# Optimization experiments

Hardware: AMD Instinct MI355X
Metric: run time of the kernel (lower is better)

Reference implementation:

```python
import jax, jax.numpy as jnp
import numpy as np

B = 32768      # batch
D = 2          # input_dim
H = 2048       # hidden_dim
NQ = 4         # qubits


def setup_inputs() -> dict:
    key = jax.random.key(0)
    ks = jax.random.split(key, 14)

    def lin(k, fan_in, fan_out):
        # kaiming-uniform-ish init like nn.Linear
        bound = 1.0 / np.sqrt(fan_in)
        kw, kb = jax.random.split(k)
        W = jax.random.uniform(kw, (fan_in, fan_out), jnp.float32, -bound, bound)
        b = jax.random.uniform(kb, (fan_out,), jnp.float32, -bound, bound)
        return W, b

    x = jax.random.normal(ks[0], (B, D), jnp.float32)
    W1, b1 = lin(ks[1], D + NQ, H)      # core Linear 1
    W2, b2 = lin(ks[2], H, H)           # core Linear 2
    Wc, bc = lin(ks[3], H, 1)           # classifier
    Wr1, br1 = lin(ks[4], D, 8)
    Wr2, br2 = lin(ks[5], 8, 4)
    Wr3, br3 = lin(ks[6], 4, 1)
    return dict(x=x, W1=W1, b1=b1, W2=W2, b2=b2, Wc=Wc, bc=bc,
                Wr1=Wr1, br1=br1, Wr2=Wr2, br2=br2, Wr3=Wr3, br3=br3)


def _quantum_feature_map(x):
    # Exact closed form of: RY(x_i) on 4 qubits from |0000>, CNOT(0,1), CNOT(2,3),
    # expval(PauliZ(i)). Padding with zeros -> cos(0)=1 on unused wires.
    xq = jnp.pad(x, ((0, 0), (0, NQ - x.shape[1])))  # [B,4]
    c = jnp.cos(xq)
    return jnp.stack([c[:, 0], c[:, 0] * c[:, 1], c[:, 2], c[:, 2] * c[:, 3]], axis=1)


def reference(x, W1, b1, W2, b2, Wc, bc, Wr1, br1, Wr2, br2, Wr3, br3):
    qfeat = _quantum_feature_map(x)               # [B,4]
    concat = jnp.concatenate([x, qfeat], axis=1)  # [B, D+4]
    h = jnp.tanh(concat @ W1 + b1)                # [B,H]
    h = jnp.tanh(h @ W2 + b2)                     # [B,H]
    logits = h @ Wc + bc                          # [B,1]
    r = jnp.tanh(x @ Wr1 + br1)
    r = jnp.tanh(r @ Wr2 + br2)
    risk = r @ Wr3 + br3                          # [B,1]
    return logits, risk
```

## Files before the change

kernel.cpp:

```cpp
#include <hip/hip_runtime.h>
#include <hip/hip_bf16.h>
#include <stdint.h>

#define B_ROWS 32768
#define HID    2048
#define K_DIM  2048

#define BM 128
#define BN 256
#define BKB 128

#define SCALE_W   5747.3639f
#define DEQUANT   1.3700225e-6f

#define L1_BLOCKS (B_ROWS / 32)
#define TR_BLOCKS ((HID/32)*(K_DIM/32))

typedef int  int4v __attribute__((ext_vector_type(4)));
typedef char char8 __attribute__((ext_vector_type(8)));

__device__ __forceinline__ float fast_tanh(float x) {
    float e = __expf(2.0f * x);
    return 1.0f - 2.0f * __builtin_amdgcn_rcpf(e + 1.0f);
}

__device__ __forceinline__ void gl_lds16(const void* g, void* l) {
    __builtin_amdgcn_global_load_lds(
        (const __attribute__((address_space(1))) void*)(uintptr_t)g,
        (__attribute__((address_space(3))) void*)(uint32_t)(uintptr_t)l,
        16, 0, 0);
}

__global__ __launch_bounds__(256) void prep_kernel(
    const float* __restrict__ x,   const float* __restrict__ W1, const float* __restrict__ b1,
    const float* __restrict__ W2,
    const float* __restrict__ Wr1, const float* __restrict__ br1,
    const float* __restrict__ Wr2, const float* __restrict__ br2,
    const float* __restrict__ Wr3, const float* __restrict__ br3,
    const float* __restrict__ bc,
    char* __restrict__ h1, char* __restrict__ W2t, float* __restrict__ out) {
    const int t = threadIdx.x;
    if (blockIdx.x >= L1_BLOCKS) {
        __shared__ float tile[32][33];
        const int tb = blockIdx.x - L1_BLOCKS;
        const int n0 = (tb & 63) * 32;
        const int k0 = (tb >> 6) * 32;
        const int tx = t & 31;
        const int ty = t >> 5;
#pragma unroll
        for (int i = 0; i < 4; ++i) {
            int k = k0 + ty + i * 8;
            tile[ty + i * 8][tx] = W2[(size_t)k * HID + n0 + tx];
        }
        __syncthreads();
#pragma unroll
        for (int i = 0; i < 4; ++i) {
            int n = n0 + ty + i * 8;
            W2t[(size_t)n * K_DIM + k0 + tx] =
                (char)__float2int_rn(tile[tx][ty + i * 8] * SCALE_W);
        }
        return;
    }
    __shared__ float4 xsh[32];
    const int brow0 = blockIdx.x * 32;
    if (t < 32) {
        const float2 xv = *(const float2*)(x + 2 * (brow0 + t));
        const float c0 = __cosf(xv.x);
        xsh[t] = float4{xv.x, xv.y, c0, c0 * __cosf(xv.y)};
    }
    const int n0 = t * 8;
    float w0[8], w1[8], w2[8], w3[8], wb[8];
#pragma unroll
    for (int j = 0; j < 8; ++j) {
        w0[j] = W1[0 * HID + n0 + j];
        w1[j] = W1[1 * HID + n0 + j];
        w2[j] = W1[2 * HID + n0 + j];
        w3[j] = W1[3 * HID + n0 + j];
        wb[j] = W1[4 * HID + n0 + j] + W1[5 * HID + n0 + j] + b1[n0 + j];
    }
    __syncthreads();
#pragma unroll 2
    for (int r = 0; r < 32; ++r) {
        const float4 xr = xsh[r];
        char8 v;
#pragma unroll
        for (int j = 0; j < 8; ++j) {
            float z = wb[j] + xr.x * w0[j] + xr.y * w1[j] + xr.z * w2[j] + xr.w * w3[j];
            v[j] = (char)__float2int_rn(fast_tanh(z) * 127.0f);
        }
        *(char8*)(h1 + (size_t)(brow0 + r) * HID + n0) = v;
    }
    if (t < 32) {
        const float x0 = xsh[t].x, x1 = xsh[t].y;
        float r1[8];
#pragma unroll
        for (int j = 0; j < 8; ++j)
            r1[j] = fast_tanh(br1[j] + x0 * Wr1[j] + x1 * Wr1[8 + j]);
        float r2[4];
#pragma unroll
        for (int j = 0; j < 4; ++j) {
            float s = br2[j];
#pragma unroll
            for (int i = 0; i < 8; ++i) s += r1[i] * Wr2[i * 4 + j];
            r2[j] = fast_tanh(s);
        }
        float risk = br3[0];
#pragma unroll
        for (int i = 0; i < 4; ++i) risk += r2[i] * Wr3[i];
        out[B_ROWS + brow0 + t] = risk;
        out[brow0 + t]          = bc[0];
    }
}

__global__ __launch_bounds__(256, 2) void gemm_kernel(
    const char* __restrict__ A,
    const char* __restrict__ Bt,
    const float* __restrict__ b2, const float* __restrict__ Wc,
    float* __restrict__ out) {
    __shared__ __align__(16) char sA[BM * BKB];
    __shared__ __align__(16) char sB[BN * BKB];

    const int tid  = threadIdx.x;
    const int wave = tid >> 6;
    const int lane = tid & 63;
    const int bid  = blockIdx.x;
    const int m0 = (bid >> 3) * BM;
    const int n0 = (bid & 7) * BN;

    const char* aSrc[4]; char* aDst[4];
    const char* bSrc[8]; char* bDst[8];
    {
        const int rsub  = lane >> 3;
        const int chunk = (lane & 7) ^ rsub;
#pragma unroll
        for (int i = 0; i < 4; ++i) {
            int seg = wave * 4 + i;
            aSrc[i] = A + (size_t)(m0 + seg * 8 + rsub) * K_DIM + chunk * 16;
            aDst[i] = sA + seg * 1024;
        }
#pragma unroll
        for (int i = 0; i < 8; ++i) {
            int seg = wave * 8 + i;
            bSrc[i] = Bt + (size_t)(n0 + seg * 8 + rsub) * K_DIM + chunk * 16;
            bDst[i] = sB + seg * 1024;
        }
    }

    int4v acc[4][8] = {};
    const int mw   = (wave & 1) * 64;
    const int nw   = (wave >> 1) * 128;
    const int quad = lane >> 4;
    const int r16  = lane & 15;
    const int x7   = lane & 7;

    for (int kb = 0; kb < K_DIM; kb += BKB) {
#pragma unroll
        for (int i = 0; i < 4; ++i) gl_lds16(aSrc[i] + kb, aDst[i]);
#pragma unroll
        for (int i = 0; i < 8; ++i) gl_lds16(bSrc[i] + kb, bDst[i]);
        __syncthreads();
#pragma unroll
        for (int ks = 0; ks < 2; ++ks) {
            const int slot = ((ks * 4 + quad) ^ x7) * 16;
            int4v af[4], bfr[8];
#pragma unroll
            for (int mi = 0; mi < 4; ++mi)
                af[mi]  = *(const int4v*)(sA + (mw + mi * 16 + r16) * BKB + slot);
#pragma unroll
            for (int ni = 0; ni < 8; ++ni)
                bfr[ni] = *(const int4v*)(sB + (nw + ni * 16 + r16) * BKB + slot);
#pragma unroll
            for (int mi = 0; mi < 4; ++mi)
#pragma unroll
                for (int ni = 0; ni < 8; ++ni)
                    acc[mi][ni] = __builtin_amdgcn_mfma_i32_16x16x64_i8(
                        af[mi], bfr[ni], acc[mi][ni], 0, 0, 0);
        }
        __syncthreads();
    }

    float b2v[8], wcv[8];
#pragma unroll
    for (int ni = 0; ni < 8; ++ni) {
        int gn = n0 + nw + ni * 16 + r16;
        b2v[ni] = b2[gn];
        wcv[ni] = Wc[gn];
    }
#pragma unroll
    for (int mi = 0; mi < 4; ++mi) {
#pragma unroll
        for (int r = 0; r < 4; ++r) {
            int gm = m0 + mw + mi * 16 + quad * 4 + r;
            float rs = 0.f;
#pragma unroll
            for (int ni = 0; ni < 8; ++ni)
                rs += fast_tanh((float)acc[mi][ni][r] * DEQUANT + b2v[ni]) * wcv[ni];
            rs += __shfl_xor(rs, 1);
            rs += __shfl_xor(rs, 2);
            rs += __shfl_xor(rs, 4);
            rs += __shfl_xor(rs, 8);
            if (r16 == 0) atomicAdd(&out[gm], rs);
        }
    }
}

extern "C" void kernel_launch(void* const* d_in, const int* in_sizes, int n_in,
                              void* d_out, int out_size, void* d_ws, size_t ws_size,
                              hipStream_t stream) {
    const float* x   = (const float*)d_in[0];
    const float* W1  = (const float*)d_in[1];
    const float* b1  = (const float*)d_in[2];
    const float* W2  = (const float*)d_in[3];
    const float* b2  = (const float*)d_in[4];
    const float* Wc  = (const float*)d_in[5];
    const float* bc  = (const float*)d_in[6];
    const float* Wr1 = (const float*)d_in[7];
    const float* br1 = (const float*)d_in[8];
    const float* Wr2 = (const float*)d_in[9];
    const float* br2 = (const float*)d_in[10];
    const float* Wr3 = (const float*)d_in[11];
    const float* br3 = (const float*)d_in[12];
    float* out = (float*)d_out;

    char* W2t = (char*)d_ws;
    char* h1  = (char*)d_ws + (size_t)4 * 1024 * 1024;

    prep_kernel<<<L1_BLOCKS + TR_BLOCKS, 256, 0, stream>>>(
        x, W1, b1, W2, Wr1, br1, Wr2, br2, Wr3, br3, bc, h1, W2t, out);
    gemm_kernel<<<(B_ROWS / BM) * (HID / BN), 256, 0, stream>>>(h1, W2t, b2, Wc, out);
}
```

Measured before the change: 260.2 us.

## Pre-tile int8 operands in MFMA fragment order and load directly to registers

The prep kernel now writes h1 and the transposed quantized W2 in a blocked layout where each 16-row by 64-byte k-slice is stored contiguously in MFMA fragment order. The GEMM then skips LDS entirely, and each lane loads its int4 fragments straight from global memory with coalesced 16-byte reads. It double-buffers registers across two k-substeps and uses scheduling barriers so the loads overlap with the MFMAs. This removes the LDS staging and the block-wide syncs, but gives up LDS-level sharing: each wave re-reads fragments from global/L2 that other waves in the block also read, so global traffic rises.

```diff
diff --git a/kernel.cpp b/kernel.cpp
--- a/kernel.cpp
+++ b/kernel.cpp
@@ -8,7 +8,7 @@
 
 #define BM 128
 #define BN 256
-#define BKB 128
+#define NKT 16
 
 #define SCALE_W   5747.3639f
 #define DEQUANT   1.3700225e-6f
@@ -18,17 +18,20 @@
 
 typedef int  int4v __attribute__((ext_vector_type(4)));
 typedef char char8 __attribute__((ext_vector_type(8)));
+
 
 __device__ __forceinline__ float fast_tanh(float x) {
     float e = __expf(2.0f * x);
     return 1.0f - 2.0f * __builtin_amdgcn_rcpf(e + 1.0f);
 }
 
-__device__ __forceinline__ void gl_lds16(const void* g, void* l) {
-    __builtin_amdgcn_global_load_lds(
-        (const __attribute__((address_space(1))) void*)(uintptr_t)g,
-        (__attribute__((address_space(3))) void*)(uint32_t)(uintptr_t)l,
-        16, 0, 0);
+#define SCHED_FENCE() __builtin_amdgcn_sched_barrier(0)
+
+__device__ __forceinline__ const char* uniform_ptr(const char* p) {
+    uint64_t v = (uint64_t)(uintptr_t)p;
+    uint32_t lo = __builtin_amdgcn_readfirstlane((uint32_t)v);
+    uint32_t hi = __builtin_amdgcn_readfirstlane((uint32_t)(v >> 32));
+    return (const char*)(uintptr_t)(((uint64_t)hi << 32) | lo);
 }
 
 __global__ __launch_bounds__(256) void prep_kernel(
@@ -53,11 +56,24 @@
             tile[ty + i * 8][tx] = W2[(size_t)k * HID + n0 + tx];
         }
         __syncthreads();
-#pragma unroll
-        for (int i = 0; i < 4; ++i) {
-            int n = n0 + ty + i * 8;
-            W2t[(size_t)n * K_DIM + k0 + tx] =
-                (char)__float2int_rn(tile[tx][ty + i * 8] * SCALE_W);
+        if (t < 64) {
+            const int n    = n0 + (t & 31);
+            const int lkq  = t >> 5;
+            const int kq64 = ((k0 >> 4) + lkq) & 3;
+            int w[4];
+#pragma unroll
+            for (int q = 0; q < 4; ++q) {
+                int v = 0;
+#pragma unroll
+                for (int j = 0; j < 4; ++j) {
+                    int c = __float2int_rn(tile[lkq * 16 + q * 4 + j][n - n0] * SCALE_W) & 255;
+                    v |= c << (8 * j);
+                }
+                w[q] = v;
+            }
+            char* dst = W2t + ((size_t)(n >> 4) * 32 + (k0 >> 6)) * 1024
+                      + ((n & 15) + (kq64 << 4)) * 16;
+            *(int4v*)dst = int4v{w[0], w[1], w[2], w[3]};
         }
         return;
     }
@@ -78,6 +94,9 @@
         w3[j] = W1[3 * HID + n0 + j];
         wb[j] = W1[4 * HID + n0 + j] + W1[5 * HID + n0 + j] + b1[n0 + j];
     }
+    const size_t kblk = (size_t)(n0 >> 6);
+    const int    kq   = (n0 >> 4) & 3;
+    const int    bofs = n0 & 15;
     __syncthreads();
 #pragma unroll 2
     for (int r = 0; r < 32; ++r) {
@@ -88,7 +107,10 @@
             float z = wb[j] + xr.x * w0[j] + xr.y * w1[j] + xr.z * w2[j] + xr.w * w3[j];
             v[j] = (char)__float2int_rn(fast_tanh(z) * 127.0f);
         }
-        *(char8*)(h1 + (size_t)(brow0 + r) * HID + n0) = v;
+        const int row = brow0 + r;
+        char* dst = h1 + ((size_t)(row >> 4) * 32 + kblk) * 1024
+                  + ((row & 15) + (kq << 4)) * 16 + bofs;
+        *(char8*)dst = v;
     }
     if (t < 32) {
         const float x0 = xsh[t].x, x1 = xsh[t].y;
@@ -117,9 +139,6 @@
     const char* __restrict__ Bt,
     const float* __restrict__ b2, const float* __restrict__ Wc,
     float* __restrict__ out) {
-    __shared__ __align__(16) char sA[BM * BKB];
-    __shared__ __align__(16) char sB[BN * BKB];
-
     const int tid  = threadIdx.x;
     const int wave = tid >> 6;
     const int lane = tid & 63;
@@ -127,56 +146,58 @@
     const int m0 = (bid >> 3) * BM;
     const int n0 = (bid & 7) * BN;
 
-    const char* aSrc[4]; char* aDst[4];
-    const char* bSrc[8]; char* bDst[8];
-    {
-        const int rsub  = lane >> 3;
-        const int chunk = (lane & 7) ^ rsub;
-#pragma unroll
-        for (int i = 0; i < 4; ++i) {
-            int seg = wave * 4 + i;
-            aSrc[i] = A + (size_t)(m0 + seg * 8 + rsub) * K_DIM + chunk * 16;
-            aDst[i] = sA + seg * 1024;
-        }
-#pragma unroll
-        for (int i = 0; i < 8; ++i) {
-            int seg = wave * 8 + i;
-            bSrc[i] = Bt + (size_t)(n0 + seg * 8 + rsub) * K_DIM + chunk * 16;
-            bDst[i] = sB + seg * 1024;
-        }
-    }
-
-    int4v acc[4][8] = {};
     const int mw   = (wave & 1) * 64;
     const int nw   = (wave >> 1) * 128;
     const int quad = lane >> 4;
     const int r16  = lane & 15;
-    const int x7   = lane & 7;
-
-    for (int kb = 0; kb < K_DIM; kb += BKB) {
-#pragma unroll
-        for (int i = 0; i < 4; ++i) gl_lds16(aSrc[i] + kb, aDst[i]);
-#pragma unroll
-        for (int i = 0; i < 8; ++i) gl_lds16(bSrc[i] + kb, bDst[i]);
-        __syncthreads();
-#pragma unroll
-        for (int ks = 0; ks < 2; ++ks) {
-            const int slot = ((ks * 4 + quad) ^ x7) * 16;
-            int4v af[4], bfr[8];
-#pragma unroll
-            for (int mi = 0; mi < 4; ++mi)
-                af[mi]  = *(const int4v*)(sA + (mw + mi * 16 + r16) * BKB + slot);
+
+    const char* aB = uniform_ptr(A  + (size_t)((m0 + mw) >> 4) * 32768);
+    const char* bB = uniform_ptr(Bt + (size_t)((n0 + nw) >> 4) * 32768);
+    uint32_t voA[4], voB[8];
+#pragma unroll
+    for (int mi = 0; mi < 4; ++mi) voA[mi] = lane * 16 + mi * 32768;
+#pragma unroll
+    for (int ni = 0; ni < 8; ++ni) voB[ni] = lane * 16 + ni * 32768;
+
+    int4v acc[4][8] = {};
+    int4v a0[4], a1[4], b0[8], b1[8];
+
+#pragma unroll
+    for (int mi = 0; mi < 4; ++mi) a0[mi] = *(const int4v*)(aB + voA[mi]);
+#pragma unroll
+    for (int ni = 0; ni < 8; ++ni) b0[ni] = *(const int4v*)(bB + voB[ni]);
+
+    for (int u = 0; u < NKT; ++u) {
+#pragma unroll
+        for (int mi = 0; mi < 4; ++mi) a1[mi] = *(const int4v*)(aB + voA[mi] + 1024);
+#pragma unroll
+        for (int ni = 0; ni < 8; ++ni) b1[ni] = *(const int4v*)(bB + voB[ni] + 1024);
+        SCHED_FENCE();
+#pragma unroll
+        for (int mi = 0; mi < 4; ++mi)
 #pragma unroll
             for (int ni = 0; ni < 8; ++ni)
-                bfr[ni] = *(const int4v*)(sB + (nw + ni * 16 + r16) * BKB + slot);
-#pragma unroll
-            for (int mi = 0; mi < 4; ++mi)
-#pragma unroll
-                for (int ni = 0; ni < 8; ++ni)
-                    acc[mi][ni] = __builtin_amdgcn_mfma_i32_16x16x64_i8(
-                        af[mi], bfr[ni], acc[mi][ni], 0, 0, 0);
-        }
-        __syncthreads();
+                acc[mi][ni] = __builtin_amdgcn_mfma_i32_16x16x64_i8(
+                    a0[mi], b0[ni], acc[mi][ni], 0, 0, 0);
+        if (u + 1 < NKT) {
+#pragma unroll
+            for (int mi = 0; mi < 4; ++mi) {
+                voA[mi] += 2048;
+                a0[mi] = *(const int4v*)(aB + voA[mi]);
+            }
+#pragma unroll
+            for (int ni = 0; ni < 8; ++ni) {
+                voB[ni] += 2048;
+                b0[ni] = *(const int4v*)(bB + voB[ni]);
+            }
+        }
+        SCHED_FENCE();
+#pragma unroll
+        for (int mi = 0; mi < 4; ++mi)
+#pragma unroll
+            for (int ni = 0; ni < 8; ++ni)
+                acc[mi][ni] = __builtin_amdgcn_mfma_i32_16x16x64_i8(
+                    a1[mi], b1[ni], acc[mi][ni], 0, 0, 0);
     }
 
     float b2v[8], wcv[8];
```

Result: faster. 253.8 us (-2.4%).
